# Kernel tuning notes

Measured on AMD Instinct MI355X. Metric: run time of the kernel, lower is better.

## Reference

```python
import jax, jax.numpy as jnp
import numpy as np

N = 100000      # nodes
E = 1600000     # edges (avg degree 16)
H = 128         # hidden_dim
V = 64          # vector_dim
NUM_LAYERS = 3


def setup_inputs() -> dict:
    key = jax.random.key(0)
    ks = jax.random.split(key, 16)
    s = 0.05
    inp = {
        "node_feats": jax.random.normal(ks[0], (N, 1), dtype=jnp.float32),
        "edge_index": jax.random.randint(ks[1], (2, E), 0, N, dtype=jnp.int64),
        "batch": jnp.zeros((N,), dtype=jnp.int64),
        "temperature": jnp.float32(1.0),
        "t": jnp.float32(1.0),
        # SAGEConv layer 0: in=1 -> out=H. PyG: lin_l (on aggregated, with bias), lin_r (on root, no bias)
        "Wl0": jax.random.normal(ks[2], (1, H), dtype=jnp.float32) * s,
        "bl0": jnp.zeros((H,), dtype=jnp.float32),
        "Wr0": jax.random.normal(ks[3], (1, H), dtype=jnp.float32) * s,
        # SAGEConv layers 1..2: H -> H, stacked
        "Wl": jax.random.normal(ks[4], (NUM_LAYERS - 1, H, H), dtype=jnp.float32) * s,
        "bl": jnp.zeros((NUM_LAYERS - 1, H), dtype=jnp.float32),
        "Wr": jax.random.normal(ks[5], (NUM_LAYERS - 1, H, H), dtype=jnp.float32) * s,
        # to_vector: H -> V
        "Wv": jax.random.normal(ks[6], (H, V), dtype=jnp.float32) * s,
        "bv": jnp.zeros((V,), dtype=jnp.float32),
        # mlp: (V+2) -> H -> 1
        "Wm1": jax.random.normal(ks[7], (V + 2, H), dtype=jnp.float32) * s,
        "bm1": jnp.zeros((H,), dtype=jnp.float32),
        "Wm2": jax.random.normal(ks[8], (H, 1), dtype=jnp.float32) * s,
        "bm2": jnp.zeros((1,), dtype=jnp.float32),
    }
    return inp


def reference(node_feats, edge_index, batch, temperature, t,
              Wl0, bl0, Wr0, Wl, bl, Wr, Wv, bv, Wm1, bm1, Wm2, bm2):
    n = node_feats.shape[0]
    src, dst = edge_index[0], edge_index[1]
    # in-degree for scatter-mean (clamp to 1 for isolated nodes, like PyG mean aggr)
    deg = jax.ops.segment_sum(jnp.ones((src.shape[0],), node_feats.dtype), dst, num_segments=n)
    deg = jnp.maximum(deg, 1.0)[:, None]  # (N,1)

    def sage(h, Wl_, bl_, Wr_):
        # scatter-mean of source features onto destination nodes
        agg = jax.ops.segment_sum(h[src], dst, num_segments=n) / deg
        return agg @ Wl_ + bl_ + h @ Wr_

    h = node_feats.reshape(-1, 1)  # (N,1)
    h = jax.nn.relu(sage(h, Wl0, bl0, Wr0))
    for i in range(Wl.shape[0]):
        h = jax.nn.relu(sage(h, Wl[i], bl[i], Wr[i]))

    # global_mean_pool over single graph (batch all zeros)
    num_graphs = 1
    cnt = jax.ops.segment_sum(jnp.ones((n,), h.dtype), batch, num_segments=num_graphs)
    pooled = jax.ops.segment_sum(h, batch, num_segments=num_graphs) / jnp.maximum(cnt, 1.0)[:, None]  # (1,H)

    z = pooled @ Wv + bv  # (1,V)  (no ReLU in original code path)
    extras = jnp.stack([jnp.asarray(temperature, z.dtype), jnp.asarray(t, z.dtype)]).reshape(1, 2)
    feat = jnp.concatenate([z, extras], axis=1)  # (1, V+2)
    out = jax.nn.softplus(jax.nn.relu(feat @ Wm1 + bm1) @ Wm2 + bm2)  # (1,1)
    return out
```

## Files before the change

kernel.cpp:

```cpp
#include <hip/hip_runtime.h>
#include <hip/hip_bf16.h>
#include <math.h>

#define H 128
#define BKT_SHIFT 9
#define BKT_NODES 512
#define CHUNK 4096
#define GEMM_GRID 512

typedef __attribute__((ext_vector_type(8))) short short8;
typedef __attribute__((ext_vector_type(4))) float f32x4;

static __device__ __forceinline__ ushort f2b(float v) {
    union { float f; unsigned u; } x; x.f = v;
    unsigned r = x.u + 0x7fffu + ((x.u >> 16) & 1u);
    return (ushort)(r >> 16);
}
static __device__ __forceinline__ float b2f(ushort b) {
    union { unsigned u; float f; } x; x.u = ((unsigned)b) << 16;
    return x.f;
}


__global__ void bucket_hist_kernel(const int* __restrict__ dst, int e,
                                   int* __restrict__ bucketCount, int* __restrict__ blockBase) {
    __shared__ int hist[256];
    int t = threadIdx.x;
    hist[t] = 0;
    __syncthreads();
    int base = blockIdx.x * CHUNK;
    #pragma unroll
    for (int k = 0; k < CHUNK / 256; k++) {
        int i = base + k * 256 + t;
        if (i < e) atomicAdd(&hist[dst[i] >> BKT_SHIFT], 1);
    }
    __syncthreads();
    blockBase[blockIdx.x * 256 + t] = atomicAdd(&bucketCount[t], hist[t]);
}

__global__ void bucket_scan_kernel(const int* __restrict__ bucketCount, int* __restrict__ bucketBase,
                                   int* __restrict__ rs, int n, int e) {
    if (threadIdx.x == 0 && blockIdx.x == 0) {
        int acc = 0;
        for (int i = 0; i < 256; i++) { bucketBase[i] = acc; acc += bucketCount[i]; }
        bucketBase[256] = acc;
        rs[n] = e;
    }
}

__global__ void bucket_scatter_kernel(const int* __restrict__ src, const int* __restrict__ dst, int e,
                                      const int* __restrict__ bucketBase, const int* __restrict__ blockBase,
                                      int2* __restrict__ grouped) {
    __shared__ int cur[256];
    int t = threadIdx.x;
    cur[t] = bucketBase[t] + blockBase[blockIdx.x * 256 + t];
    __syncthreads();
    int base = blockIdx.x * CHUNK;
    #pragma unroll
    for (int k = 0; k < CHUNK / 256; k++) {
        int i = base + k * 256 + t;
        if (i < e) {
            int d = dst[i];
            int pos = atomicAdd(&cur[d >> BKT_SHIFT], 1);
            int2 p; p.x = d; p.y = src[i];
            grouped[pos] = p;
        }
    }
}

__global__ void bucket_csr_kernel(const int2* __restrict__ grouped, const int* __restrict__ bucketBase,
                                  int* __restrict__ rs, int* __restrict__ csr, int n) {
    __shared__ int sdeg[BKT_NODES];
    __shared__ int sexcl[BKT_NODES];
    __shared__ int wsum[4];
    int b = blockIdx.x;
    int t = threadIdx.x;
    int nodeBase = b << BKT_SHIFT;
    int ebase = bucketBase[b], eend = bucketBase[b + 1];
    sdeg[t] = 0; sdeg[t + 256] = 0;
    __syncthreads();
    for (int e = ebase + t; e < eend; e += 256)
        atomicAdd(&sdeg[grouped[e].x - nodeBase], 1);
    __syncthreads();
    int lane = t & 63, wid = t >> 6;
    int v0 = sdeg[2 * t], v1 = sdeg[2 * t + 1];
    int p = v0 + v1;
    int x = p;
    #pragma unroll
    for (int off = 1; off < 64; off <<= 1) {
        int y = __shfl_up(x, off, 64);
        if (lane >= off) x += y;
    }
    if (lane == 63) wsum[wid] = x;
    __syncthreads();
    if (t == 0) {
        int acc = 0;
        #pragma unroll
        for (int w = 0; w < 4; w++) { int tmp = wsum[w]; wsum[w] = acc; acc += tmp; }
    }
    __syncthreads();
    int basep = wsum[wid] + x - p;
    sexcl[2 * t] = basep;
    sexcl[2 * t + 1] = basep + v0;
    int nodes = min(BKT_NODES, n - nodeBase);
    for (int i = t; i < nodes; i += 256) rs[nodeBase + i] = ebase + sexcl[i];
    sdeg[t] = 0; sdeg[t + 256] = 0;
    __syncthreads();
    for (int e = ebase + t; e < eend; e += 256) {
        int2 pr = grouped[e];
        int l = pr.x - nodeBase;
        int r = atomicAdd(&sdeg[l], 1);
        csr[ebase + sexcl[l] + r] = pr.y;
    }
}


__global__ void prep_w_kernel(const float* __restrict__ Wl, const float* __restrict__ Wr,
                              ushort* __restrict__ Btg) {
    int idx = blockIdx.x * 256 + threadIdx.x;
    if (idx >= 65536) return;
    int l = idx >> 15;
    int col = (idx >> 8) & 127;
    int k = idx & 255;
    float v = (k < 128) ? Wl[l * H * H + k * H + col] : Wr[l * H * H + (k - 128) * H + col];
    Btg[idx] = f2b(v);
}


__global__ void agg0_kernel(const float* __restrict__ x, const int* __restrict__ rs,
                            const int* __restrict__ csr, float* __restrict__ agg0, int n) {
    int i = blockIdx.x * 256 + threadIdx.x;
    if (i >= n) return;
    int a = rs[i], b = rs[i + 1];
    float s = 0.f;
    for (int e = a; e < b; e++) s += x[csr[e]];
    agg0[i] = s / (float)max(b - a, 1);
}

__global__ void expand0_kernel(const float* __restrict__ x, const float* __restrict__ agg0,
                               const float* __restrict__ Wl0, const float* __restrict__ bl0,
                               const float* __restrict__ Wr0, ushort* __restrict__ hout, int n) {
    int idx = blockIdx.x * 256 + threadIdx.x;
    if (idx >= n * H) return;
    int i = idx >> 7, j = idx & (H - 1);
    float v = agg0[i] * Wl0[j] + bl0[j] + x[i] * Wr0[j];
    hout[idx] = f2b(fmaxf(v, 0.f));
}


__global__ void aggregate_kernel(const ushort* __restrict__ hb, const int* __restrict__ rs,
                                 const int* __restrict__ csr, ushort* __restrict__ aggb, int n) {
    int node = blockIdx.x * 4 + (threadIdx.x >> 6);
    int lane = threadIdx.x & 63;
    if (node >= n) return;
    int g = lane >> 4;
    int fl = lane & 15;
    int a = rs[node], b = rs[node + 1];
    float s[8] = {0.f, 0.f, 0.f, 0.f, 0.f, 0.f, 0.f, 0.f};
    int e = a;
    for (; e + 8 <= b; e += 8) {
        int n0 = csr[e + g], n1 = csr[e + 4 + g];
        short8 v0 = *(const short8*)(hb + (size_t)n0 * H + 8 * fl);
        short8 v1 = *(const short8*)(hb + (size_t)n1 * H + 8 * fl);
        #pragma unroll
        for (int j = 0; j < 8; j++) s[j] += b2f((ushort)v0[j]) + b2f((ushort)v1[j]);
    }
    for (; e + 4 <= b; e += 4) {
        int n0 = csr[e + g];
        short8 v0 = *(const short8*)(hb + (size_t)n0 * H + 8 * fl);
        #pragma unroll
        for (int j = 0; j < 8; j++) s[j] += b2f((ushort)v0[j]);
    }
    if (e < b && g < (b - e)) {
        int n0 = csr[e + g];
        short8 v0 = *(const short8*)(hb + (size_t)n0 * H + 8 * fl);
        #pragma unroll
        for (int j = 0; j < 8; j++) s[j] += b2f((ushort)v0[j]);
    }
    #pragma unroll
    for (int j = 0; j < 8; j++) {
        s[j] += __shfl_xor(s[j], 16, 64);
        s[j] += __shfl_xor(s[j], 32, 64);
    }
    if (lane < 16) {
        float inv = 1.f / (float)max(b - a, 1);
        short8 o;
        #pragma unroll
        for (int j = 0; j < 8; j++) o[j] = (short)f2b(s[j] * inv);
        *(short8*)(aggb + (size_t)node * H + 8 * fl) = o;
    }
}


template<bool POOL>
__global__ __launch_bounds__(256, 2) void gemm_kernel(
    const ushort* __restrict__ aggb, const ushort* __restrict__ hb,
    const ushort* __restrict__ Btg,
    const float* __restrict__ bias, ushort* __restrict__ out,
    float* __restrict__ partial, int nblk, int n) {
    __shared__ float sums[2][128];
    int tid = threadIdx.x;
    int wave = tid >> 6, lane = tid & 63;
    int l15 = lane & 15, lhi = lane >> 4;
    int colhalf = wave & 1;
    int rowsub = wave >> 1;
    int colbase = colhalf * 64;

    short8 bf[4][8];
    #pragma unroll
    for (int c2 = 0; c2 < 4; c2++) {
        const ushort* wp = Btg + (colbase + c2 * 16 + l15) * 256 + lhi * 8;
        #pragma unroll
        for (int s = 0; s < 8; s++)
            bf[c2][s] = *(const short8*)(wp + s * 32);
    }
    f32x4 bias_v[4];
    #pragma unroll
    for (int c2 = 0; c2 < 4; c2++)
        bias_v[c2] = *(const f32x4*)(bias + colbase + c2 * 16 + lhi * 4);

    f32x4 fs[4];
    #pragma unroll
    for (int c2 = 0; c2 < 4; c2++) fs[c2] = (f32x4){0.f, 0.f, 0.f, 0.f};

    for (int r0 = blockIdx.x * 32; r0 < n; r0 += nblk * 32) {
        int row = r0 + rowsub * 16 + l15;
        int arow = min(row, n - 1);
        short8 af[8];
        #pragma unroll
        for (int s = 0; s < 8; s++)
            af[s] = *(const short8*)((s < 4 ? aggb : hb) + (size_t)arow * H + (s & 3) * 32 + lhi * 8);
        f32x4 acc[4];
        #pragma unroll
        for (int c2 = 0; c2 < 4; c2++) acc[c2] = (f32x4){0.f, 0.f, 0.f, 0.f};
        #pragma unroll
        for (int s = 0; s < 8; s++) {
            #pragma unroll
            for (int c2 = 0; c2 < 4; c2++)
                acc[c2] = __builtin_amdgcn_mfma_f32_16x16x32_bf16(bf[c2][s], af[s], acc[c2], 0, 0, 0);
        }
        if (row < n) {
            if (POOL) {
                #pragma unroll
                for (int c2 = 0; c2 < 4; c2++)
                    #pragma unroll
                    for (int r = 0; r < 4; r++)
                        fs[c2][r] += fmaxf(acc[c2][r] + bias_v[c2][r], 0.f);
            } else {
                #pragma unroll
                for (int c2 = 0; c2 < 4; c2++) {
                    ushort4 o;
                    o.x = f2b(fmaxf(acc[c2][0] + bias_v[c2][0], 0.f));
                    o.y = f2b(fmaxf(acc[c2][1] + bias_v[c2][1], 0.f));
                    o.z = f2b(fmaxf(acc[c2][2] + bias_v[c2][2], 0.f));
                    o.w = f2b(fmaxf(acc[c2][3] + bias_v[c2][3], 0.f));
                    *(ushort4*)(out + (size_t)row * H + colbase + c2 * 16 + lhi * 4) = o;
                }
            }
        }
    }

    if (POOL) {
        #pragma unroll
        for (int c2 = 0; c2 < 4; c2++) {
            #pragma unroll
            for (int m = 1; m < 16; m <<= 1) {
                #pragma unroll
                for (int r = 0; r < 4; r++)
                    fs[c2][r] += __shfl_xor(fs[c2][r], m, 64);
            }
        }
        if (l15 == 0) {
            #pragma unroll
            for (int c2 = 0; c2 < 4; c2++)
                #pragma unroll
                for (int r = 0; r < 4; r++)
                    sums[rowsub][colbase + c2 * 16 + lhi * 4 + r] = fs[c2][r];
        }
        __syncthreads();
        if (tid < 128)
            partial[tid * nblk + blockIdx.x] = sums[0][tid] + sums[1][tid];
    }
}


__global__ void pool_reduce_kernel(const float* __restrict__ partial, float* __restrict__ pooled,
                                   int nb, float invn) {
    int j = blockIdx.x;
    int t = threadIdx.x;
    float s = 0.f;
    for (int b = t; b < nb; b += 64) s += partial[j * nb + b];
    #pragma unroll
    for (int off = 32; off > 0; off >>= 1) s += __shfl_down(s, off, 64);
    if (t == 0) pooled[j] = s * invn;
}


__global__ void mlp_kernel(const float* __restrict__ pooled,
                           const float* __restrict__ Wv, const float* __restrict__ bv,
                           const float* __restrict__ temp, const float* __restrict__ tt,
                           const float* __restrict__ Wm1, const float* __restrict__ bm1,
                           const float* __restrict__ Wm2, const float* __restrict__ bm2,
                           float* __restrict__ out) {
    __shared__ float feat[66];
    __shared__ float red[2];
    int j = threadIdx.x;
    if (j < 64) {
        float s = bv[j];
        for (int k = 0; k < H; k++) s += pooled[k] * Wv[k * 64 + j];
        feat[j] = s;
    }
    if (j == 64) feat[64] = temp[0];
    if (j == 65) feat[65] = tt[0];
    __syncthreads();
    float m = bm1[j];
    for (int k = 0; k < 66; k++) m += feat[k] * Wm1[k * H + j];
    m = fmaxf(m, 0.f);
    float p = m * Wm2[j];
    #pragma unroll
    for (int off = 32; off > 0; off >>= 1) p += __shfl_down(p, off, 64);
    if ((j & 63) == 0) red[j >> 6] = p;
    __syncthreads();
    if (j == 0) {
        float x = red[0] + red[1] + bm2[0];
        out[0] = (x > 20.f) ? x : log1pf(expf(x));
    }
}


extern "C" void kernel_launch(void* const* d_in, const int* in_sizes, int n_in,
                              void* d_out, int out_size, void* d_ws, size_t ws_size,
                              hipStream_t stream) {
    const float* node_feats = (const float*)d_in[0];
    const int* edge_index = (const int*)d_in[1];
    const float* temp = (const float*)d_in[3];
    const float* tt   = (const float*)d_in[4];
    const float* Wl0 = (const float*)d_in[5];
    const float* bl0 = (const float*)d_in[6];
    const float* Wr0 = (const float*)d_in[7];
    const float* Wl  = (const float*)d_in[8];
    const float* bl  = (const float*)d_in[9];
    const float* Wr  = (const float*)d_in[10];
    const float* Wv  = (const float*)d_in[11];
    const float* bv  = (const float*)d_in[12];
    const float* Wm1 = (const float*)d_in[13];
    const float* bm1 = (const float*)d_in[14];
    const float* Wm2 = (const float*)d_in[15];
    const float* bm2 = (const float*)d_in[16];

    const int N = in_sizes[0];
    const int E = in_sizes[1] / 2;
    const int* src = edge_index;
    const int* dst = edge_index + E;

    size_t NH = (size_t)N * H;
    ushort* hA   = (ushort*)d_ws;
    ushort* hB   = hA + NH;
    ushort* aggb = hB + NH;
    ushort* Btg  = aggb + NH;
    float* agg0  = (float*)(Btg + 65536);
    int2* grouped = (int2*)(agg0 + N);
    int* csr     = (int*)(grouped + E);
    int* rs      = csr + E;
    int* bucketCount = rs + (N + 1);
    int* bucketBase  = bucketCount + 256;
    int* blockBase   = bucketBase + 257;
    int NBLK = (E + CHUNK - 1) / CHUNK;
    float* partial = (float*)(blockBase + NBLK * 256);
    float* pooled  = partial + (size_t)H * GEMM_GRID;

    int NB = (N + BKT_NODES - 1) / BKT_NODES;

    hipMemsetAsync(bucketCount, 0, 256 * sizeof(int), stream);
    bucket_hist_kernel<<<NBLK, 256, 0, stream>>>(dst, E, bucketCount, blockBase);
    bucket_scan_kernel<<<1, 64, 0, stream>>>(bucketCount, bucketBase, rs, N, E);
    bucket_scatter_kernel<<<NBLK, 256, 0, stream>>>(src, dst, E, bucketBase, blockBase, grouped);
    bucket_csr_kernel<<<NB, 256, 0, stream>>>(grouped, bucketBase, rs, csr, N);

    prep_w_kernel<<<256, 256, 0, stream>>>(Wl, Wr, Btg);

    agg0_kernel<<<(N + 255) / 256, 256, 0, stream>>>(node_feats, rs, csr, agg0, N);
    expand0_kernel<<<((size_t)N * H + 255) / 256, 256, 0, stream>>>(node_feats, agg0, Wl0, bl0, Wr0, hA, N);

    aggregate_kernel<<<(N + 3) / 4, 256, 0, stream>>>(hA, rs, csr, aggb, N);
    gemm_kernel<false><<<GEMM_GRID, 256, 0, stream>>>(aggb, hA, Btg, bl, hB, nullptr, GEMM_GRID, N);

    aggregate_kernel<<<(N + 3) / 4, 256, 0, stream>>>(hB, rs, csr, aggb, N);
    gemm_kernel<true><<<GEMM_GRID, 256, 0, stream>>>(aggb, hB, Btg + 32768, bl + H, nullptr, partial, GEMM_GRID, N);

    pool_reduce_kernel<<<H, 64, 0, stream>>>(partial, pooled, GEMM_GRID, 1.0f / (float)N);
    mlp_kernel<<<1, H, 0, stream>>>(pooled, Wv, bv, temp, tt, Wm1, bm1, Wm2, bm2, (float*)d_out);
}
```

Before: 278.2 us.

## Gather neighbor features from an FP8 copy of hidden states in aggregation

Producers (expand0 and the first GEMM) now also write a scaled FP8 copy of the hidden state. The aggregation kernel gathers neighbor rows from that copy, halving the bytes per random row fetch, and handles two nodes per wave with 32 lanes each. Sums are still accumulated in fp32 and rescaled when the mean is taken. The cost is extra FP8 writes, lower precision in the aggregated features, and reuse of the grouped buffer for the FP8 copy; CHUNK is also halved for the bucketing kernels.

```diff
diff --git a/kernel.cpp b/kernel.cpp
--- a/kernel.cpp
+++ b/kernel.cpp
@@ -5,11 +5,14 @@
 #define H 128
 #define BKT_SHIFT 9
 #define BKT_NODES 512
-#define CHUNK 4096
+#define CHUNK 2048
 #define GEMM_GRID 512
+#define FP8_SCALE 64.0f
+#define FP8_INV (1.0f / 64.0f)
 
 typedef __attribute__((ext_vector_type(8))) short short8;
 typedef __attribute__((ext_vector_type(4))) float f32x4;
+typedef __attribute__((ext_vector_type(2))) float f32x2;
 
 static __device__ __forceinline__ ushort f2b(float v) {
     union { float f; unsigned u; } x; x.f = v;
@@ -139,55 +142,92 @@
 
 __global__ void expand0_kernel(const float* __restrict__ x, const float* __restrict__ agg0,
                                const float* __restrict__ Wl0, const float* __restrict__ bl0,
-                               const float* __restrict__ Wr0, ushort* __restrict__ hout, int n) {
+                               const float* __restrict__ Wr0, ushort* __restrict__ hout,
+                               ushort* __restrict__ h8, int n) {
     int idx = blockIdx.x * 256 + threadIdx.x;
-    if (idx >= n * H) return;
-    int i = idx >> 7, j = idx & (H - 1);
-    float v = agg0[i] * Wl0[j] + bl0[j] + x[i] * Wr0[j];
-    hout[idx] = f2b(fmaxf(v, 0.f));
-}
-
-
-__global__ void aggregate_kernel(const ushort* __restrict__ hb, const int* __restrict__ rs,
-                                 const int* __restrict__ csr, ushort* __restrict__ aggb, int n) {
-    int node = blockIdx.x * 4 + (threadIdx.x >> 6);
-    int lane = threadIdx.x & 63;
+    if (idx >= n * 64) return;
+    int i = idx >> 6, j = (idx & 63) * 2;
+    float gi = agg0[i], xi = x[i];
+    float v0 = fmaxf(gi * Wl0[j] + bl0[j] + xi * Wr0[j], 0.f);
+    float v1 = fmaxf(gi * Wl0[j + 1] + bl0[j + 1] + xi * Wr0[j + 1], 0.f);
+    ushort2 o; o.x = f2b(v0); o.y = f2b(v1);
+    *(ushort2*)(hout + (size_t)i * H + j) = o;
+    int p = __builtin_amdgcn_cvt_pk_fp8_f32(v0 * FP8_SCALE, v1 * FP8_SCALE, 0, false);
+    h8[(size_t)i * 64 + (idx & 63)] = (ushort)p;
+}
+
+
+__global__ void aggregate8_kernel(const unsigned char* __restrict__ h8, const int* __restrict__ rs,
+                                  const int* __restrict__ csr, ushort* __restrict__ aggb, int n) {
+    int tid = threadIdx.x;
+    int w = (tid >> 5) & 1;
+    int node = blockIdx.x * 8 + (tid >> 6) * 2 + w;
     if (node >= n) return;
-    int g = lane >> 4;
-    int fl = lane & 15;
+    int sl = (tid >> 3) & 3;
+    int fl = tid & 7;
     int a = rs[node], b = rs[node + 1];
-    float s[8] = {0.f, 0.f, 0.f, 0.f, 0.f, 0.f, 0.f, 0.f};
+    f32x2 s[8];
+    #pragma unroll
+    for (int j = 0; j < 8; j++) s[j] = (f32x2){0.f, 0.f};
+
     int e = a;
     for (; e + 8 <= b; e += 8) {
-        int n0 = csr[e + g], n1 = csr[e + 4 + g];
-        short8 v0 = *(const short8*)(hb + (size_t)n0 * H + 8 * fl);
-        short8 v1 = *(const short8*)(hb + (size_t)n1 * H + 8 * fl);
-        #pragma unroll
-        for (int j = 0; j < 8; j++) s[j] += b2f((ushort)v0[j]) + b2f((ushort)v1[j]);
+        int n0 = csr[e + sl], n1 = csr[e + 4 + sl];
+        uint4 u0 = *(const uint4*)(h8 + (size_t)n0 * 128 + 16 * fl);
+        uint4 u1 = *(const uint4*)(h8 + (size_t)n1 * 128 + 16 * fl);
+        unsigned dw[8] = {u0.x, u0.y, u0.z, u0.w, u1.x, u1.y, u1.z, u1.w};
+        #pragma unroll
+        for (int d = 0; d < 8; d++) {
+            f32x2 lo = __builtin_amdgcn_cvt_pk_f32_fp8(dw[d], false);
+            f32x2 hi = __builtin_amdgcn_cvt_pk_f32_fp8(dw[d], true);
+            s[(d & 3) * 2] += lo;
+            s[(d & 3) * 2 + 1] += hi;
+        }
     }
     for (; e + 4 <= b; e += 4) {
-        int n0 = csr[e + g];
-        short8 v0 = *(const short8*)(hb + (size_t)n0 * H + 8 * fl);
-        #pragma unroll
-        for (int j = 0; j < 8; j++) s[j] += b2f((ushort)v0[j]);
-    }
-    if (e < b && g < (b - e)) {
-        int n0 = csr[e + g];
-        short8 v0 = *(const short8*)(hb + (size_t)n0 * H + 8 * fl);
-        #pragma unroll
-        for (int j = 0; j < 8; j++) s[j] += b2f((ushort)v0[j]);
+        int n0 = csr[e + sl];
+        uint4 u0 = *(const uint4*)(h8 + (size_t)n0 * 128 + 16 * fl);
+        unsigned dw[4] = {u0.x, u0.y, u0.z, u0.w};
+        #pragma unroll
+        for (int d = 0; d < 4; d++) {
+            f32x2 lo = __builtin_amdgcn_cvt_pk_f32_fp8(dw[d], false);
+            f32x2 hi = __builtin_amdgcn_cvt_pk_f32_fp8(dw[d], true);
+            s[d * 2] += lo;
+            s[d * 2 + 1] += hi;
+        }
+    }
+    if (e < b && sl < (b - e)) {
+        int n0 = csr[e + sl];
+        uint4 u0 = *(const uint4*)(h8 + (size_t)n0 * 128 + 16 * fl);
+        unsigned dw[4] = {u0.x, u0.y, u0.z, u0.w};
+        #pragma unroll
+        for (int d = 0; d < 4; d++) {
+            f32x2 lo = __builtin_amdgcn_cvt_pk_f32_fp8(dw[d], false);
+            f32x2 hi = __builtin_amdgcn_cvt_pk_f32_fp8(dw[d], true);
+            s[d * 2] += lo;
+            s[d * 2 + 1] += hi;
+        }
     }
     #pragma unroll
     for (int j = 0; j < 8; j++) {
-        s[j] += __shfl_xor(s[j], 16, 64);
-        s[j] += __shfl_xor(s[j], 32, 64);
-    }
-    if (lane < 16) {
-        float inv = 1.f / (float)max(b - a, 1);
-        short8 o;
-        #pragma unroll
-        for (int j = 0; j < 8; j++) o[j] = (short)f2b(s[j] * inv);
-        *(short8*)(aggb + (size_t)node * H + 8 * fl) = o;
+        s[j].x += __shfl_xor(s[j].x, 8, 64);
+        s[j].y += __shfl_xor(s[j].y, 8, 64);
+        s[j].x += __shfl_xor(s[j].x, 16, 64);
+        s[j].y += __shfl_xor(s[j].y, 16, 64);
+    }
+    if (sl == 0) {
+        float inv = FP8_INV / (float)max(b - a, 1);
+        short8 o0, o1;
+        #pragma unroll
+        for (int j = 0; j < 4; j++) {
+            o0[2 * j]     = (short)f2b(s[j].x * inv);
+            o0[2 * j + 1] = (short)f2b(s[j].y * inv);
+            o1[2 * j]     = (short)f2b(s[j + 4].x * inv);
+            o1[2 * j + 1] = (short)f2b(s[j + 4].y * inv);
+        }
+        ushort* dstp = aggb + (size_t)node * H + 16 * fl;
+        *(short8*)dstp = o0;
+        *(short8*)(dstp + 8) = o1;
     }
 }
 
@@ -197,6 +237,7 @@
     const ushort* __restrict__ aggb, const ushort* __restrict__ hb,
     const ushort* __restrict__ Btg,
     const float* __restrict__ bias, ushort* __restrict__ out,
+    unsigned char* __restrict__ out8,
     float* __restrict__ partial, int nblk, int n) {
     __shared__ float sums[2][128];
     int tid = threadIdx.x;
@@ -249,12 +290,16 @@
             } else {
                 #pragma unroll
                 for (int c2 = 0; c2 < 4; c2++) {
+                    float v0 = fmaxf(acc[c2][0] + bias_v[c2][0], 0.f);
+                    float v1 = fmaxf(acc[c2][1] + bias_v[c2][1], 0.f);
+                    float v2 = fmaxf(acc[c2][2] + bias_v[c2][2], 0.f);
+                    float v3 = fmaxf(acc[c2][3] + bias_v[c2][3], 0.f);
                     ushort4 o;
-                    o.x = f2b(fmaxf(acc[c2][0] + bias_v[c2][0], 0.f));
-                    o.y = f2b(fmaxf(acc[c2][1] + bias_v[c2][1], 0.f));
-                    o.z = f2b(fmaxf(acc[c2][2] + bias_v[c2][2], 0.f));
-                    o.w = f2b(fmaxf(acc[c2][3] + bias_v[c2][3], 0.f));
+                    o.x = f2b(v0); o.y = f2b(v1); o.z = f2b(v2); o.w = f2b(v3);
                     *(ushort4*)(out + (size_t)row * H + colbase + c2 * 16 + lhi * 4) = o;
+                    int p = __builtin_amdgcn_cvt_pk_fp8_f32(v0 * FP8_SCALE, v1 * FP8_SCALE, 0, false);
+                    p = __builtin_amdgcn_cvt_pk_fp8_f32(v2 * FP8_SCALE, v3 * FP8_SCALE, p, true);
+                    *(unsigned int*)(out8 + (size_t)row * 128 + colbase + c2 * 16 + lhi * 4) = (unsigned)p;
                 }
             }
         }
@@ -368,6 +413,8 @@
     int NBLK = (E + CHUNK - 1) / CHUNK;
     float* partial = (float*)(blockBase + NBLK * 256);
     float* pooled  = partial + (size_t)H * GEMM_GRID;
+    unsigned char* hB8 = (unsigned char*)(pooled + H);
+    unsigned char* hA8 = (unsigned char*)grouped;
 
     int NB = (N + BKT_NODES - 1) / BKT_NODES;
 
@@ -380,13 +427,14 @@
     prep_w_kernel<<<256, 256, 0, stream>>>(Wl, Wr, Btg);
 
     agg0_kernel<<<(N + 255) / 256, 256, 0, stream>>>(node_feats, rs, csr, agg0, N);
-    expand0_kernel<<<((size_t)N * H + 255) / 256, 256, 0, stream>>>(node_feats, agg0, Wl0, bl0, Wr0, hA, N);
-
-    aggregate_kernel<<<(N + 3) / 4, 256, 0, stream>>>(hA, rs, csr, aggb, N);
-    gemm_kernel<false><<<GEMM_GRID, 256, 0, stream>>>(aggb, hA, Btg, bl, hB, nullptr, GEMM_GRID, N);
-
-    aggregate_kernel<<<(N + 3) / 4, 256, 0, stream>>>(hB, rs, csr, aggb, N);
-    gemm_kernel<true><<<GEMM_GRID, 256, 0, stream>>>(aggb, hB, Btg + 32768, bl + H, nullptr, partial, GEMM_GRID, N);
+    expand0_kernel<<<((size_t)N * 64 + 255) / 256, 256, 0, stream>>>(
+        node_feats, agg0, Wl0, bl0, Wr0, hA, (ushort*)hA8, N);
+
+    aggregate8_kernel<<<(N + 7) / 8, 256, 0, stream>>>(hA8, rs, csr, aggb, N);
+    gemm_kernel<false><<<GEMM_GRID, 256, 0, stream>>>(aggb, hA, Btg, bl, hB, hB8, nullptr, GEMM_GRID, N);
+
+    aggregate8_kernel<<<(N + 7) / 8, 256, 0, stream>>>(hB8, rs, csr, aggb, N);
+    gemm_kernel<true><<<GEMM_GRID, 256, 0, stream>>>(aggb, hB, Btg + 32768, bl + H, nullptr, nullptr, partial, GEMM_GRID, N);
 
     pool_reduce_kernel<<<H, 64, 0, stream>>>(partial, pooled, GEMM_GRID, 1.0f / (float)N);
     mlp_kernel<<<1, H, 0, stream>>>(pooled, Wv, bv, temp, tt, Wm1, bm1, Wm2, bm2, (float*)d_out);
```

New measurement: 259.4 us. 6.8% less time.
